# Kernel tuning notes

Measured on AMD Instinct MI355X. Metric: run time of the kernel, lower is better.

The kernel has to match this reference:

```python
import jax, jax.numpy as jnp
import numpy as np

N = 100000      # nodes
E = 1600000     # edges
DIM = 64        # feat_channel
H = 4           # heads
C = DIM // H    # per-head channels
L = 3           # layer_num
G = 16          # graphs in batch
NCLS = 2
NEG_SLOPE_ATT = 0.2   # GATConv leaky relu
NEG_SLOPE_ACT = 0.01  # 'Leaky' activation
EPS = 1e-5


def setup_inputs() -> dict:
    key = jax.random.key(0)
    ks = jax.random.split(key, 8)
    x = jax.random.normal(ks[0], (N, DIM), dtype=jnp.float32)
    edge_index = jax.random.randint(ks[1], (2, E), 0, N, dtype=jnp.int32)
    batch = jnp.sort(jax.random.randint(ks[2], (N,), 0, G, dtype=jnp.int32))
    W = jax.random.normal(ks[3], (L, DIM, DIM), dtype=jnp.float32) / np.sqrt(DIM)
    att_src = jax.random.normal(ks[4], (L, H, C), dtype=jnp.float32) * 0.1
    att_dst = jax.random.normal(ks[5], (L, H, C), dtype=jnp.float32) * 0.1
    bias = jnp.zeros((L, DIM), dtype=jnp.float32)
    gamma = jnp.ones((L, DIM), dtype=jnp.float32)
    beta = jnp.zeros((L, DIM), dtype=jnp.float32)
    Wr = jax.random.normal(ks[6], ((L + 1) * DIM, NCLS), dtype=jnp.float32) / np.sqrt((L + 1) * DIM)
    br = jnp.zeros((NCLS,), dtype=jnp.float32)
    return {"x": x, "edge_index": edge_index, "batch": batch, "n_graphs": G,
            "W": W, "att_src": att_src, "att_dst": att_dst, "bias": bias,
            "gamma": gamma, "beta": beta, "Wr": Wr, "br": br}


def _gat_conv(x, src, dst, W_l, a_src, a_dst, b_l):
    # x: [N, DIM] -> h: [N, H, C]
    h = (x @ W_l).reshape(-1, H, C)
    # per-node attention logits [N, H]
    e_src = jnp.einsum('nhc,hc->nh', h, a_src)
    e_dst = jnp.einsum('nhc,hc->nh', h, a_dst)
    alpha = jax.nn.leaky_relu(e_src[src] + e_dst[dst], NEG_SLOPE_ATT)  # [E, H]
    # segment softmax over incoming edges of each destination node
    amax = jax.ops.segment_max(alpha, dst, num_segments=N)
    ex = jnp.exp(alpha - amax[dst])
    den = jax.ops.segment_sum(ex, dst, num_segments=N)
    att = ex / (den[dst] + 1e-16)                                      # [E, H]
    # weighted scatter aggregation
    msg = h[src] * att[:, :, None]                                     # [E, H, C]
    out = jax.ops.segment_sum(msg, dst, num_segments=N)
    return out.reshape(-1, H * C) + b_l, att


def _batch_norm(x, g, b):
    mu = jnp.mean(x, axis=0)
    var = jnp.var(x, axis=0)
    return (x - mu) * jax.lax.rsqrt(var + EPS) * g + b


def _mean_pool(x, batch, n_graphs, cnt):
    return jax.ops.segment_sum(x, batch, num_segments=n_graphs) / cnt[:, None]


def reference(x, edge_index, batch, n_graphs, W, att_src, att_dst, bias, gamma, beta, Wr, br):
    src, dst = edge_index[0], edge_index[1]
    cnt = jax.ops.segment_sum(jnp.ones((x.shape[0],), x.dtype), batch,
                              num_segments=n_graphs)                   # nodes per graph
    inv_sqrt_n = jax.lax.rsqrt(cnt)[batch][:, None]                    # GraphSizeNorm factor

    x_out = x
    pools = [_mean_pool(x, batch, n_graphs, cnt)]                      # x0_glob
    for l in range(L):
        h, _att = _gat_conv(x_out, src, dst, W[l], att_src[l], att_dst[l], bias[l])
        h = _batch_norm(h, gamma[l], beta[l]) * inv_sqrt_n             # BatchNorm + GraphSizeNorm
        h = jax.nn.leaky_relu(h, NEG_SLOPE_ACT)
        pools.append(_mean_pool(h, batch, n_graphs, cnt))
        x_out = h + x_out                                              # residual 'Y'

    x_concat = jnp.concatenate(pools, axis=1)                          # [G, (L+1)*DIM]
    risk = x_concat @ Wr + br                                          # [G, NCLS]
    Y_prob = jax.nn.softmax(risk, axis=1)
    Y_hat = jnp.argmax(risk, axis=1)
    return risk, Y_prob, Y_hat
```

## Files before the change

### kernel.cpp

```cpp
#include <hip/hip_runtime.h>

constexpr int NN   = 100000;
constexpr int EE   = 1600000;
constexpr int DIM  = 64;
constexpr int HH   = 4;
constexpr int CC   = 16;
constexpr int LL   = 3;
constexpr int GG   = 16;
constexpr int NCLS = 2;
constexpr float SLOPE_ATT = 0.2f;
constexpr float SLOPE_ACT = 0.01f;
constexpr float EPS = 1e-5f;

constexpr int SCAN_CHUNK = 1024;
constexpr int NSCAN = (NN + SCAN_CHUNK - 1) / SCAN_CHUNK;
constexpr int NREP = 64;

typedef int vint4 __attribute__((ext_vector_type(4)));

__device__ __forceinline__ float lrelu_att(float v) { return v > 0.f ? v : SLOPE_ATT * v; }
__device__ __forceinline__ float lrelu_act(float v) { return v > 0.f ? v : SLOPE_ACT * v; }

__device__ __forceinline__ unsigned short f2bf(float f) {
    unsigned u = __float_as_uint(f);
    unsigned r = u + 0x7FFFu + ((u >> 16) & 1u);
    return (unsigned short)(r >> 16);
}
__device__ __forceinline__ float bflo(unsigned u) { return __uint_as_float(u << 16); }
__device__ __forceinline__ float bfhi(unsigned u) { return __uint_as_float(u & 0xFFFF0000u); }

__global__ __launch_bounds__(256) void k_hist(const int* __restrict__ ei,
                                              int* __restrict__ deg) {
    int i = blockIdx.x * 256 + threadIdx.x;
    if (i < EE / 4) {
        vint4 d = __builtin_nontemporal_load(&((const vint4*)(ei + EE))[i]);
        atomicAdd(&deg[d.x], 1);
        atomicAdd(&deg[d.y], 1);
        atomicAdd(&deg[d.z], 1);
        atomicAdd(&deg[d.w], 1);
    }
}

__global__ __launch_bounds__(256) void k_scan1(const int* __restrict__ deg,
                                               int* __restrict__ excl,
                                               int* __restrict__ bsum) {
    __shared__ int sh[256];
    const int b = blockIdx.x, t = threadIdx.x;
    const int i0 = b * SCAN_CHUNK + t * 4;
    int v[4];
#pragma unroll
    for (int i = 0; i < 4; ++i) v[i] = (i0 + i < NN) ? deg[i0 + i] : 0;
    int tsum = v[0] + v[1] + v[2] + v[3];
    sh[t] = tsum;
    __syncthreads();
    for (int o = 1; o < 256; o <<= 1) {
        int x = (t >= o) ? sh[t - o] : 0;
        __syncthreads();
        sh[t] += x;
        __syncthreads();
    }
    if (t == 255) bsum[b] = sh[255];
    int run = sh[t] - tsum;
#pragma unroll
    for (int i = 0; i < 4; ++i) {
        if (i0 + i < NN) excl[i0 + i] = run;
        run += v[i];
    }
}

__global__ void k_scan2(const int* __restrict__ bsum, int* __restrict__ bsum_sc) {
    __shared__ int sh[128];
    const int t = threadIdx.x;
    const int own = (t < NSCAN) ? bsum[t] : 0;
    sh[t] = own;
    __syncthreads();
    for (int o = 1; o < 128; o <<= 1) {
        int x = (t >= o) ? sh[t - o] : 0;
        __syncthreads();
        sh[t] += x;
        __syncthreads();
    }
    if (t < NSCAN) bsum_sc[t] = sh[t] - own;
}

__global__ __launch_bounds__(256) void k_scan3(int* __restrict__ row_start,
                                               const int* __restrict__ bsum_sc,
                                               int* __restrict__ cursor) {
    int i = blockIdx.x * 256 + threadIdx.x;
    if (i < NN) {
        int v = row_start[i] + bsum_sc[i / SCAN_CHUNK];
        row_start[i] = v;
        cursor[i] = v;
    }
    if (i == 0) row_start[NN] = EE;
}

constexpr int FILL_NBLK = 256;
constexpr int DRANGE = (NN + 7) / 8;
__global__ __launch_bounds__(256) void k_fill(const int* __restrict__ ei,
                                              int* __restrict__ cursor,
                                              int* __restrict__ ssrc) {
    const int g = blockIdx.x & 7;
    const int blk = blockIdx.x >> 3;
    const int dlo = g * DRANGE, dhi = min(dlo + DRANGE, NN);
    const int stride = FILL_NBLK * 256;
    for (int e = blk * 256 + threadIdx.x; e < EE; e += stride) {
        int d = __builtin_nontemporal_load(&ei[EE + e]);
        if (d >= dlo && d < dhi) {
            int s = __builtin_nontemporal_load(&ei[e]);
            int pos = atomicAdd(&cursor[d], 1);
            ssrc[pos] = s;
        }
    }
}

template<int MODE>
__global__ __launch_bounds__(256) void k_gemm_t(const float* __restrict__ xbase,
                                                const float* __restrict__ aggin,
                                                const float* __restrict__ scshf,
                                                const int* __restrict__ batch,
                                                const float* __restrict__ cntin,
                                                const float* __restrict__ Wl,
                                                const float* __restrict__ asrc,
                                                const float* __restrict__ adst,
                                                float* __restrict__ xcur_out,
                                                unsigned short* __restrict__ h,
                                                float* __restrict__ es,
                                                float* __restrict__ ed,
                                                double* __restrict__ bnrep,
                                                float* __restrict__ poolout,
                                                float* __restrict__ cntout) {
    if (blockIdx.x < NREP && threadIdx.x < 128)
        bnrep[(size_t)blockIdx.x * 128 + threadIdx.x] = 0.0;
    __shared__ float Ws[DIM][DIM];
    __shared__ float xsT[DIM][DIM];
    __shared__ float sp[GG * 64];
    __shared__ float scnt[GG];
    const int tid = threadIdx.x;
    const int row0 = blockIdx.x * 64;

    for (int i = tid; i < GG * 64; i += 256) sp[i] = 0.f;
    if (MODE == 0 && tid < GG) scnt[tid] = 0.f;
    __syncthreads();

    const float4* W4 = (const float4*)Wl;
#pragma unroll
    for (int i = 0; i < 4; ++i) ((float4*)Ws)[tid + 256 * i] = W4[tid + 256 * i];

    const int c4_ = tid & 15;
    float4 scv, shfv;
    if (MODE == 1) {
        scv  = ((const float4*)scshf)[c4_];
        shfv = ((const float4*)scshf)[16 + c4_];
    }

#pragma unroll
    for (int i = 0; i < 4; ++i) {
        int idx4 = tid + 256 * i;
        int r = idx4 >> 4, c4 = idx4 & 15;
        int grow = row0 + r;
        float4 v4 = make_float4(0.f, 0.f, 0.f, 0.f);
        if (grow < NN) {
            if (MODE == 0) {
                v4 = ((const float4*)xbase)[grow * 16 + c4];
                int g = batch[grow];
                atomicAdd(&sp[g * 64 + c4 * 4 + 0], v4.x);
                atomicAdd(&sp[g * 64 + c4 * 4 + 1], v4.y);
                atomicAdd(&sp[g * 64 + c4 * 4 + 2], v4.z);
                atomicAdd(&sp[g * 64 + c4 * 4 + 3], v4.w);
                if (c4 == 0) atomicAdd(&scnt[g], 1.f);
            } else {
                float4 a4 = ((const float4*)aggin)[grow * 16 + c4];
                float4 xb = ((const float4*)xbase)[grow * 16 + c4];
                int g = batch[grow];
                float rinv = rsqrtf(cntin[g]);
                float vx = lrelu_act((a4.x * scv.x + shfv.x) * rinv);
                float vy = lrelu_act((a4.y * scv.y + shfv.y) * rinv);
                float vz = lrelu_act((a4.z * scv.z + shfv.z) * rinv);
                float vw = lrelu_act((a4.w * scv.w + shfv.w) * rinv);
                atomicAdd(&sp[g * 64 + c4 * 4 + 0], vx);
                atomicAdd(&sp[g * 64 + c4 * 4 + 1], vy);
                atomicAdd(&sp[g * 64 + c4 * 4 + 2], vz);
                atomicAdd(&sp[g * 64 + c4 * 4 + 3], vw);
                v4 = make_float4(xb.x + vx, xb.y + vy, xb.z + vz, xb.w + vw);
                ((float4*)xcur_out)[grow * 16 + c4] = v4;
            }
        }
        int col = (((r >> 2) ^ c4) << 2) | (r & 3);
        xsT[c4 * 4 + 0][col] = v4.x;
        xsT[c4 * 4 + 1][col] = v4.y;
        xsT[c4 * 4 + 2][col] = v4.z;
        xsT[c4 * 4 + 3][col] = v4.w;
    }
    __syncthreads();

    const int tc = tid & 15, tr = tid >> 4;
    float acc[4][4] = {};
#pragma unroll 8
    for (int k = 0; k < DIM; ++k) {
        int kc = (k >> 2) & 15;
        float4 wv = *(const float4*)(&Ws[k][tc * 4]);
        float4 xv = *(const float4*)(&xsT[k][(tr ^ kc) * 4]);
        acc[0][0] = fmaf(xv.x, wv.x, acc[0][0]);
        acc[0][1] = fmaf(xv.x, wv.y, acc[0][1]);
        acc[0][2] = fmaf(xv.x, wv.z, acc[0][2]);
        acc[0][3] = fmaf(xv.x, wv.w, acc[0][3]);
        acc[1][0] = fmaf(xv.y, wv.x, acc[1][0]);
        acc[1][1] = fmaf(xv.y, wv.y, acc[1][1]);
        acc[1][2] = fmaf(xv.y, wv.z, acc[1][2]);
        acc[1][3] = fmaf(xv.y, wv.w, acc[1][3]);
        acc[2][0] = fmaf(xv.z, wv.x, acc[2][0]);
        acc[2][1] = fmaf(xv.z, wv.y, acc[2][1]);
        acc[2][2] = fmaf(xv.z, wv.z, acc[2][2]);
        acc[2][3] = fmaf(xv.z, wv.w, acc[2][3]);
        acc[3][0] = fmaf(xv.w, wv.x, acc[3][0]);
        acc[3][1] = fmaf(xv.w, wv.y, acc[3][1]);
        acc[3][2] = fmaf(xv.w, wv.z, acc[3][2]);
        acc[3][3] = fmaf(xv.w, wv.w, acc[3][3]);
    }

    float a_s[4], a_d[4];
#pragma unroll
    for (int c = 0; c < 4; ++c) { a_s[c] = asrc[4 * tc + c]; a_d[c] = adst[4 * tc + c]; }

#pragma unroll
    for (int r = 0; r < 4; ++r) {
        int n = row0 + 4 * tr + r;
        if (n < NN) {
            ushort4 hb;
            hb.x = f2bf(acc[r][0]); hb.y = f2bf(acc[r][1]);
            hb.z = f2bf(acc[r][2]); hb.w = f2bf(acc[r][3]);
            *(ushort4*)(h + n * 64 + 4 * tc) = hb;
            float ps = acc[r][0] * a_s[0] + acc[r][1] * a_s[1] +
                       acc[r][2] * a_s[2] + acc[r][3] * a_s[3];
            float pd = acc[r][0] * a_d[0] + acc[r][1] * a_d[1] +
                       acc[r][2] * a_d[2] + acc[r][3] * a_d[3];
            ps += __shfl_xor(ps, 1); ps += __shfl_xor(ps, 2);
            pd += __shfl_xor(pd, 1); pd += __shfl_xor(pd, 2);
            if ((tc & 3) == 0) {
                es[n * 4 + (tc >> 2)] = ps;
                ed[n * 4 + (tc >> 2)] = pd;
            }
        }
    }

    for (int i = tid; i < GG * 64; i += 256)
        if (sp[i] != 0.f) atomicAdd(&poolout[i], sp[i]);
    if (MODE == 0 && tid < GG && scnt[tid] != 0.f) atomicAdd(&cntout[tid], scnt[tid]);
}

__global__ __launch_bounds__(256) void k_gat_agg(const int* __restrict__ row_start,
                                                 const int* __restrict__ ssrc,
                                                 const float* __restrict__ es,
                                                 const float* __restrict__ ed,
                                                 const unsigned short* __restrict__ h,
                                                 float* __restrict__ agg,
                                                 double* __restrict__ bnrep) {
    __shared__ int   sbuf[16][34];
    __shared__ float exbuf[16][34][4];
    __shared__ float stS[4][64];
    __shared__ float stQ[4][64];

    const int lane16 = threadIdx.x & 15;
    const int grp    = threadIdx.x >> 4;
    const int wid    = threadIdx.x >> 6;
    const int sub    = lane16 >> 3;
    const int l8     = lane16 & 7;
    const int hq8    = l8 >> 1;
    const int n = blockIdx.x * 16 + grp;
    const int base = row_start[n];
    const int deg  = row_start[n + 1] - base;
    const float4 edv = *(const float4*)(ed + n * 4);
    const uint4* h16 = (const uint4*)h;

    float acc8[8] = {};
    float4 denp = make_float4(0.f, 0.f, 0.f, 0.f);

    if (deg <= 32) {
        int s0 = 0, s1 = 0;
        float4 al0 = make_float4(-INFINITY, -INFINITY, -INFINITY, -INFINITY);
        float4 al1 = al0;
        if (lane16 < deg) {
            s0 = ssrc[base + lane16];
            float4 ev = *(const float4*)(es + s0 * 4);
            al0.x = lrelu_att(ev.x + edv.x); al0.y = lrelu_att(ev.y + edv.y);
            al0.z = lrelu_att(ev.z + edv.z); al0.w = lrelu_att(ev.w + edv.w);
        }
        if (lane16 + 16 < deg) {
            s1 = ssrc[base + 16 + lane16];
            float4 ev = *(const float4*)(es + s1 * 4);
            al1.x = lrelu_att(ev.x + edv.x); al1.y = lrelu_att(ev.y + edv.y);
            al1.z = lrelu_att(ev.z + edv.z); al1.w = lrelu_att(ev.w + edv.w);
        }
        float4 mx = make_float4(fmaxf(al0.x, al1.x), fmaxf(al0.y, al1.y),
                                fmaxf(al0.z, al1.z), fmaxf(al0.w, al1.w));
#pragma unroll
        for (int o = 1; o < 16; o <<= 1) {
            mx.x = fmaxf(mx.x, __shfl_xor(mx.x, o));
            mx.y = fmaxf(mx.y, __shfl_xor(mx.y, o));
            mx.z = fmaxf(mx.z, __shfl_xor(mx.z, o));
            mx.w = fmaxf(mx.w, __shfl_xor(mx.w, o));
        }
        float4 ex0 = make_float4(0.f, 0.f, 0.f, 0.f), ex1 = ex0;
        if (lane16 < deg) {
            ex0.x = __expf(al0.x - mx.x); ex0.y = __expf(al0.y - mx.y);
            ex0.z = __expf(al0.z - mx.z); ex0.w = __expf(al0.w - mx.w);
        }
        if (lane16 + 16 < deg) {
            ex1.x = __expf(al1.x - mx.x); ex1.y = __expf(al1.y - mx.y);
            ex1.z = __expf(al1.z - mx.z); ex1.w = __expf(al1.w - mx.w);
        }
        denp.x = ex0.x + ex1.x; denp.y = ex0.y + ex1.y;
        denp.z = ex0.z + ex1.z; denp.w = ex0.w + ex1.w;
        sbuf[grp][lane16] = s0;
        sbuf[grp][lane16 + 16] = s1;
        *(float4*)&exbuf[grp][lane16][0] = ex0;
        *(float4*)&exbuf[grp][lane16 + 16][0] = ex1;
        const int dceil = (deg + 1) & ~1;
#pragma unroll 4
        for (int i = 0; i < dceil; i += 2) {
            int si = sbuf[grp][i + sub];
            float e = exbuf[grp][i + sub][hq8];
            uint4 hv = h16[si * 8 + l8];
            acc8[0] = fmaf(e, bflo(hv.x), acc8[0]);
            acc8[1] = fmaf(e, bfhi(hv.x), acc8[1]);
            acc8[2] = fmaf(e, bflo(hv.y), acc8[2]);
            acc8[3] = fmaf(e, bfhi(hv.y), acc8[3]);
            acc8[4] = fmaf(e, bflo(hv.z), acc8[4]);
            acc8[5] = fmaf(e, bfhi(hv.z), acc8[5]);
            acc8[6] = fmaf(e, bflo(hv.w), acc8[6]);
            acc8[7] = fmaf(e, bfhi(hv.w), acc8[7]);
        }
    } else {
        float4 mx = make_float4(-INFINITY, -INFINITY, -INFINITY, -INFINITY);
        for (int c0 = 0; c0 < deg; c0 += 16) {
            if (c0 + lane16 < deg) {
                int s = ssrc[base + c0 + lane16];
                float4 ev = *(const float4*)(es + s * 4);
                mx.x = fmaxf(mx.x, lrelu_att(ev.x + edv.x));
                mx.y = fmaxf(mx.y, lrelu_att(ev.y + edv.y));
                mx.z = fmaxf(mx.z, lrelu_att(ev.z + edv.z));
                mx.w = fmaxf(mx.w, lrelu_att(ev.w + edv.w));
            }
        }
#pragma unroll
        for (int o = 1; o < 16; o <<= 1) {
            mx.x = fmaxf(mx.x, __shfl_xor(mx.x, o));
            mx.y = fmaxf(mx.y, __shfl_xor(mx.y, o));
            mx.z = fmaxf(mx.z, __shfl_xor(mx.z, o));
            mx.w = fmaxf(mx.w, __shfl_xor(mx.w, o));
        }
        for (int c0 = 0; c0 < deg; c0 += 16) {
            int cn = min(16, deg - c0);
            float4 ex = make_float4(0.f, 0.f, 0.f, 0.f);
            int s = 0;
            if (lane16 < cn) {
                s = ssrc[base + c0 + lane16];
                float4 ev = *(const float4*)(es + s * 4);
                ex.x = __expf(lrelu_att(ev.x + edv.x) - mx.x);
                ex.y = __expf(lrelu_att(ev.y + edv.y) - mx.y);
                ex.z = __expf(lrelu_att(ev.z + edv.z) - mx.z);
                ex.w = __expf(lrelu_att(ev.w + edv.w) - mx.w);
            }
            denp.x += ex.x; denp.y += ex.y; denp.z += ex.z; denp.w += ex.w;
            sbuf[grp][lane16] = s;
            *(float4*)&exbuf[grp][lane16][0] = ex;
            const int pc = (cn + 1) & ~1;
            for (int i = 0; i < pc; i += 2) {
                int si = sbuf[grp][i + sub];
                float e = exbuf[grp][i + sub][hq8];
                uint4 hv = h16[si * 8 + l8];
                acc8[0] = fmaf(e, bflo(hv.x), acc8[0]);
                acc8[1] = fmaf(e, bfhi(hv.x), acc8[1]);
                acc8[2] = fmaf(e, bflo(hv.y), acc8[2]);
                acc8[3] = fmaf(e, bfhi(hv.y), acc8[3]);
                acc8[4] = fmaf(e, bflo(hv.z), acc8[4]);
                acc8[5] = fmaf(e, bfhi(hv.z), acc8[5]);
                acc8[6] = fmaf(e, bflo(hv.w), acc8[6]);
                acc8[7] = fmaf(e, bfhi(hv.w), acc8[7]);
            }
        }
    }

#pragma unroll
    for (int q = 0; q < 8; ++q) acc8[q] += __shfl_xor(acc8[q], 8);
#pragma unroll
    for (int o = 1; o < 16; o <<= 1) {
        denp.x += __shfl_xor(denp.x, o);
        denp.y += __shfl_xor(denp.y, o);
        denp.z += __shfl_xor(denp.z, o);
        denp.w += __shfl_xor(denp.w, o);
    }
    float dh = hq8 == 0 ? denp.x : hq8 == 1 ? denp.y : hq8 == 2 ? denp.z : denp.w;
    float inv = 1.f / (dh + 1e-16f);
    float o8[8];
#pragma unroll
    for (int q = 0; q < 8; ++q) o8[q] = acc8[q] * inv;

    if (sub == 0) {
        *(float4*)(agg + n * 64 + l8 * 8)     = make_float4(o8[0], o8[1], o8[2], o8[3]);
        *(float4*)(agg + n * 64 + l8 * 8 + 4) = make_float4(o8[4], o8[5], o8[6], o8[7]);
    }

    float sv[8], qv[8];
#pragma unroll
    for (int q = 0; q < 8; ++q) {
        float v = (sub == 0) ? o8[q] : 0.f;
        sv[q] = v; qv[q] = v * v;
    }
#pragma unroll
    for (int q = 0; q < 8; ++q) {
        sv[q] += __shfl_xor(sv[q], 16); sv[q] += __shfl_xor(sv[q], 32);
        qv[q] += __shfl_xor(qv[q], 16); qv[q] += __shfl_xor(qv[q], 32);
    }
    if ((threadIdx.x & 63) < 8) {
        *(float4*)&stS[wid][l8 * 8]     = make_float4(sv[0], sv[1], sv[2], sv[3]);
        *(float4*)&stS[wid][l8 * 8 + 4] = make_float4(sv[4], sv[5], sv[6], sv[7]);
        *(float4*)&stQ[wid][l8 * 8]     = make_float4(qv[0], qv[1], qv[2], qv[3]);
        *(float4*)&stQ[wid][l8 * 8 + 4] = make_float4(qv[4], qv[5], qv[6], qv[7]);
    }
    __syncthreads();
    if (threadIdx.x < 64) {
        int j = threadIdx.x;
        float ssum = stS[0][j] + stS[1][j] + stS[2][j] + stS[3][j];
        float qsum = stQ[0][j] + stQ[1][j] + stQ[2][j] + stQ[3][j];
        double* rep = bnrep + (size_t)(blockIdx.x & (NREP - 1)) * 128;
        atomicAdd(&rep[j], (double)ssum);
        atomicAdd(&rep[64 + j], (double)qsum);
    }
}

__global__ void k_bn_final(const double* __restrict__ bnrep,
                           const float* __restrict__ gamma,
                           const float* __restrict__ beta,
                           float* __restrict__ scshf) {
    int j = threadIdx.x;
    if (j < 64) {
        double s1 = 0.0, s2 = 0.0;
        for (int rp = 0; rp < NREP; ++rp) {
            s1 += bnrep[(size_t)rp * 128 + j];
            s2 += bnrep[(size_t)rp * 128 + 64 + j];
        }
        double mean = s1 / (double)NN;
        double var = s2 / (double)NN - mean * mean;
        float sc = (float)(1.0 / sqrt(var + (double)EPS)) * gamma[j];
        scshf[j] = sc;
        scshf[64 + j] = beta[j] - (float)mean * sc;
    }
}

constexpr int NA_BLOCKS = 512;
constexpr int NA_NODES = (NN + NA_BLOCKS - 1) / NA_BLOCKS;
__global__ __launch_bounds__(256) void k_pool_final(const float* __restrict__ agg,
                                                    const float* __restrict__ scshf,
                                                    const int* __restrict__ batch,
                                                    const float* __restrict__ cnt,
                                                    float* __restrict__ pool) {
    __shared__ float sp[GG * 64];
    for (int i = threadIdx.x; i < GG * 64; i += 256) sp[i] = 0.f;
    __syncthreads();
    const int j = threadIdx.x & 63, r = threadIdx.x >> 6;
    const float sc = scshf[j], shf = scshf[64 + j];
    const int n0 = blockIdx.x * NA_NODES;
    const int n1 = min(n0 + NA_NODES, NN);
    float racc = 0.f;
    int curg = -1;
    float rinv = 0.f;
    for (int n = n0 + r; n < n1; n += 4) {
        int g = batch[n];
        if (g != curg) {
            if (curg >= 0) atomicAdd(&sp[curg * 64 + j], racc);
            curg = g; racc = 0.f;
            rinv = rsqrtf(cnt[g]);
        }
        float v = (agg[n * 64 + j] * sc + shf) * rinv;
        racc += lrelu_act(v);
    }
    if (curg >= 0) atomicAdd(&sp[curg * 64 + j], racc);
    __syncthreads();
    for (int i = threadIdx.x; i < GG * 64; i += 256)
        if (sp[i] != 0.f) atomicAdd(&pool[i], sp[i]);
}

__global__ void k_head(const float* __restrict__ pools,
                       const float* __restrict__ cnt,
                       const float* __restrict__ Wr,
                       const float* __restrict__ br,
                       float* __restrict__ out) {
    __shared__ float risk[GG * NCLS];
    int t = threadIdx.x;
    if (t < GG * NCLS) {
        int g = t / NCLS, c = t % NCLS;
        float acc = br[c];
        float icnt = 1.f / cnt[g];
        for (int k = 0; k < (LL + 1) * DIM; ++k) {
            int l = k >> 6, j = k & 63;
            float xc = pools[(l * GG + g) * 64 + j] * icnt;
            acc += xc * Wr[k * NCLS + c];
        }
        risk[t] = acc;
        out[t] = acc;
    }
    __syncthreads();
    if (t < GG) {
        float r0 = risk[t * 2], r1 = risk[t * 2 + 1];
        float m = fmaxf(r0, r1);
        float e0 = expf(r0 - m), e1 = expf(r1 - m);
        float s = e0 + e1;
        out[GG * NCLS + t * 2] = e0 / s;
        out[GG * NCLS + t * 2 + 1] = e1 / s;
        out[2 * GG * NCLS + t] = (r1 > r0) ? 1.f : 0.f;
    }
}

extern "C" void kernel_launch(void* const* d_in, const int* in_sizes, int n_in,
                              void* d_out, int out_size, void* d_ws, size_t ws_size,
                              hipStream_t stream) {
    const float* x     = (const float*)d_in[0];
    const int*   ei    = (const int*)d_in[1];
    const int*   batch = (const int*)d_in[2];
    const float* W     = (const float*)d_in[4];
    const float* asrc  = (const float*)d_in[5];
    const float* adst  = (const float*)d_in[6];
    const float* gamma = (const float*)d_in[8];
    const float* beta  = (const float*)d_in[9];
    const float* Wr    = (const float*)d_in[10];
    const float* br    = (const float*)d_in[11];
    float* out = (float*)d_out;

    char* ws = (char*)d_ws;
    size_t off = 0;
    auto alloc = [&](size_t bytes) {
        void* p = ws + off;
        off += (bytes + 255) & ~(size_t)255;
        return p;
    };
    float*          xcur      = (float*)alloc((size_t)NN * 64 * 4);
    unsigned short* h         = (unsigned short*)alloc((size_t)NN * 64 * 2);
    float*          agg       = (float*)alloc((size_t)NN * 64 * 4);
    float*          es        = (float*)alloc((size_t)NN * 4 * 4);
    float*          ed        = (float*)alloc((size_t)NN * 4 * 4);
    int*            row_start = (int*)alloc((size_t)(NN + 1) * 4);
    int*            ssrc      = (int*)alloc((size_t)EE * 4);
    double*         bnrep     = (double*)alloc((size_t)NREP * 128 * 8);
    float*          scshf     = (float*)alloc(128 * 4);
    float*          pools     = (float*)alloc((size_t)(LL + 1) * GG * 64 * 4);
    float*          cnt       = (float*)alloc((size_t)GG * 4);
    (void)ws_size; (void)in_sizes; (void)n_in; (void)out_size;

    int* deg     = (int*)agg;
    int* cursor  = (int*)agg + NN;
    int* bsum    = (int*)agg + 2 * NN;
    int* bsum_sc = (int*)agg + 2 * NN + 256;

    hipMemsetAsync(pools, 0, (size_t)(LL + 1) * GG * 64 * 4, stream);
    hipMemsetAsync(cnt, 0, (size_t)GG * 4, stream);
    hipMemsetAsync(deg, 0, (size_t)NN * 4, stream);

    k_hist<<<(EE / 4 + 255) / 256, 256, 0, stream>>>(ei, deg);
    k_scan1<<<NSCAN, 256, 0, stream>>>(deg, row_start, bsum);
    k_scan2<<<1, 128, 0, stream>>>(bsum, bsum_sc);
    k_scan3<<<(NN + 255) / 256, 256, 0, stream>>>(row_start, bsum_sc, cursor);
    k_fill<<<8 * FILL_NBLK, 256, 0, stream>>>(ei, cursor, ssrc);

    const int GEMM_GRID = (NN + 63) / 64;

    k_gemm_t<0><<<GEMM_GRID, 256, 0, stream>>>(x, nullptr, nullptr, batch, nullptr,
                                               W, asrc, adst, nullptr,
                                               h, es, ed, bnrep, pools, cnt);
    k_gat_agg<<<NN / 16, 256, 0, stream>>>(row_start, ssrc, es, ed, h, agg, bnrep);
    k_bn_final<<<1, 64, 0, stream>>>(bnrep, gamma, beta, scshf);

    k_gemm_t<1><<<GEMM_GRID, 256, 0, stream>>>(x, agg, scshf, batch, cnt,
                                               W + DIM * DIM, asrc + HH * CC, adst + HH * CC,
                                               xcur, h, es, ed, bnrep,
                                               pools + GG * 64, nullptr);
    k_gat_agg<<<NN / 16, 256, 0, stream>>>(row_start, ssrc, es, ed, h, agg, bnrep);
    k_bn_final<<<1, 64, 0, stream>>>(bnrep, gamma + DIM, beta + DIM, scshf);

    k_gemm_t<1><<<GEMM_GRID, 256, 0, stream>>>(xcur, agg, scshf, batch, cnt,
                                               W + 2 * DIM * DIM, asrc + 2 * HH * CC,
                                               adst + 2 * HH * CC,
                                               xcur, h, es, ed, bnrep,
                                               pools + 2 * GG * 64, nullptr);
    k_gat_agg<<<NN / 16, 256, 0, stream>>>(row_start, ssrc, es, ed, h, agg, bnrep);
    k_bn_final<<<1, 64, 0, stream>>>(bnrep, gamma + 2 * DIM, beta + 2 * DIM, scshf);

    k_pool_final<<<NA_BLOCKS, 256, 0, stream>>>(agg, scshf, batch, cnt,
                                                pools + 3 * GG * 64);

    k_head<<<1, 64, 0, stream>>>(pools, cnt, Wr, br, out);
}
```

Before: 595.4 us.

## Record edge ranks in histogram, fuse scan passes, skip unused residual write

```diff
diff --git a/kernel.cpp b/kernel.cpp
--- a/kernel.cpp
+++ b/kernel.cpp
@@ -30,14 +30,17 @@
 __device__ __forceinline__ float bfhi(unsigned u) { return __uint_as_float(u & 0xFFFF0000u); }
 
 __global__ __launch_bounds__(256) void k_hist(const int* __restrict__ ei,
-                                              int* __restrict__ deg) {
+                                              int* __restrict__ deg,
+                                              int* __restrict__ rank) {
     int i = blockIdx.x * 256 + threadIdx.x;
     if (i < EE / 4) {
         vint4 d = __builtin_nontemporal_load(&((const vint4*)(ei + EE))[i]);
-        atomicAdd(&deg[d.x], 1);
-        atomicAdd(&deg[d.y], 1);
-        atomicAdd(&deg[d.z], 1);
-        atomicAdd(&deg[d.w], 1);
+        vint4 r;
+        r.x = atomicAdd(&deg[d.x], 1);
+        r.y = atomicAdd(&deg[d.y], 1);
+        r.z = atomicAdd(&deg[d.z], 1);
+        r.w = atomicAdd(&deg[d.w], 1);
+        __builtin_nontemporal_store(r, &((vint4*)rank)[i]);
     }
 }
 
@@ -68,37 +71,30 @@
     }
 }
 
-__global__ void k_scan2(const int* __restrict__ bsum, int* __restrict__ bsum_sc) {
+__global__ __launch_bounds__(256) void k_scan23(int* __restrict__ row_start,
+                                                const int* __restrict__ bsum) {
     __shared__ int sh[128];
+    __shared__ int prefix;
     const int t = threadIdx.x;
-    const int own = (t < NSCAN) ? bsum[t] : 0;
-    sh[t] = own;
-    __syncthreads();
-    for (int o = 1; o < 128; o <<= 1) {
-        int x = (t >= o) ? sh[t - o] : 0;
-        __syncthreads();
-        sh[t] += x;
-        __syncthreads();
-    }
-    if (t < NSCAN) bsum_sc[t] = sh[t] - own;
-}
-
-__global__ __launch_bounds__(256) void k_scan3(int* __restrict__ row_start,
-                                               const int* __restrict__ bsum_sc,
-                                               int* __restrict__ cursor) {
-    int i = blockIdx.x * 256 + threadIdx.x;
-    if (i < NN) {
-        int v = row_start[i] + bsum_sc[i / SCAN_CHUNK];
-        row_start[i] = v;
-        cursor[i] = v;
-    }
+    if (t < NSCAN) sh[t] = bsum[t];
+    __syncthreads();
+    if (t == 0) {
+        int ci = blockIdx.x >> 2;
+        int p = 0;
+        for (int k = 0; k < ci; ++k) p += sh[k];
+        prefix = p;
+    }
+    __syncthreads();
+    int i = blockIdx.x * 256 + t;
+    if (i < NN) row_start[i] = row_start[i] + prefix;
     if (i == 0) row_start[NN] = EE;
 }
 
 constexpr int FILL_NBLK = 256;
 constexpr int DRANGE = (NN + 7) / 8;
 __global__ __launch_bounds__(256) void k_fill(const int* __restrict__ ei,
-                                              int* __restrict__ cursor,
+                                              const int* __restrict__ rank,
+                                              const int* __restrict__ row_start,
                                               int* __restrict__ ssrc) {
     const int g = blockIdx.x & 7;
     const int blk = blockIdx.x >> 3;
@@ -108,8 +104,8 @@
         int d = __builtin_nontemporal_load(&ei[EE + e]);
         if (d >= dlo && d < dhi) {
             int s = __builtin_nontemporal_load(&ei[e]);
-            int pos = atomicAdd(&cursor[d], 1);
-            ssrc[pos] = s;
+            int r = __builtin_nontemporal_load(&rank[e]);
+            ssrc[row_start[d] + r] = s;
         }
     }
 }
@@ -149,7 +145,7 @@
 
     const int c4_ = tid & 15;
     float4 scv, shfv;
-    if (MODE == 1) {
+    if (MODE >= 1) {
         scv  = ((const float4*)scshf)[c4_];
         shfv = ((const float4*)scshf)[16 + c4_];
     }
@@ -183,7 +179,7 @@
                 atomicAdd(&sp[g * 64 + c4 * 4 + 2], vz);
                 atomicAdd(&sp[g * 64 + c4 * 4 + 3], vw);
                 v4 = make_float4(xb.x + vx, xb.y + vy, xb.z + vz, xb.w + vw);
-                ((float4*)xcur_out)[grow * 16 + c4] = v4;
+                if (MODE == 1) ((float4*)xcur_out)[grow * 16 + c4] = v4;
             }
         }
         int col = (((r >> 2) ^ c4) << 2) | (r & 3);
@@ -546,22 +542,19 @@
     float*          scshf     = (float*)alloc(128 * 4);
     float*          pools     = (float*)alloc((size_t)(LL + 1) * GG * 64 * 4);
     float*          cnt       = (float*)alloc((size_t)GG * 4);
+    int*            deg       = (int*)alloc((size_t)NN * 4);
     (void)ws_size; (void)in_sizes; (void)n_in; (void)out_size;
 
-    int* deg     = (int*)agg;
-    int* cursor  = (int*)agg + NN;
-    int* bsum    = (int*)agg + 2 * NN;
-    int* bsum_sc = (int*)agg + 2 * NN + 256;
-
-    hipMemsetAsync(pools, 0, (size_t)(LL + 1) * GG * 64 * 4, stream);
-    hipMemsetAsync(cnt, 0, (size_t)GG * 4, stream);
-    hipMemsetAsync(deg, 0, (size_t)NN * 4, stream);
-
-    k_hist<<<(EE / 4 + 255) / 256, 256, 0, stream>>>(ei, deg);
+    int* bsum = (int*)agg;
+    int* rank = (int*)agg + 1024;
+
+    hipMemsetAsync(pools, 0,
+                   (size_t)(LL + 1) * GG * 64 * 4 + 256 + (size_t)NN * 4, stream);
+
+    k_hist<<<(EE / 4 + 255) / 256, 256, 0, stream>>>(ei, deg, rank);
     k_scan1<<<NSCAN, 256, 0, stream>>>(deg, row_start, bsum);
-    k_scan2<<<1, 128, 0, stream>>>(bsum, bsum_sc);
-    k_scan3<<<(NN + 255) / 256, 256, 0, stream>>>(row_start, bsum_sc, cursor);
-    k_fill<<<8 * FILL_NBLK, 256, 0, stream>>>(ei, cursor, ssrc);
+    k_scan23<<<(NN + 255) / 256, 256, 0, stream>>>(row_start, bsum);
+    k_fill<<<8 * FILL_NBLK, 256, 0, stream>>>(ei, rank, row_start, ssrc);
 
     const int GEMM_GRID = (NN + 63) / 64;
 
@@ -578,10 +571,10 @@
     k_gat_agg<<<NN / 16, 256, 0, stream>>>(row_start, ssrc, es, ed, h, agg, bnrep);
     k_bn_final<<<1, 64, 0, stream>>>(bnrep, gamma + DIM, beta + DIM, scshf);
 
-    k_gemm_t<1><<<GEMM_GRID, 256, 0, stream>>>(xcur, agg, scshf, batch, cnt,
+    k_gemm_t<2><<<GEMM_GRID, 256, 0, stream>>>(xcur, agg, scshf, batch, cnt,
                                                W + 2 * DIM * DIM, asrc + 2 * HH * CC,
                                                adst + 2 * HH * CC,
-                                               xcur, h, es, ed, bnrep,
+                                               nullptr, h, es, ed, bnrep,
                                                pools + 2 * GG * 64, nullptr);
     k_gat_agg<<<NN / 16, 256, 0, stream>>>(row_start, ssrc, es, ed, h, agg, bnrep);
     k_bn_final<<<1, 64, 0, stream>>>(bnrep, gamma + 2 * DIM, beta + 2 * DIM, scshf);
```

Result: faster. 562.6 us (-5.5%).
